# Kernel optimization log

Measured on AMD Instinct MI355X. Metric: run time of the kernel, lower is better.

## Reference

```python
import jax, jax.numpy as jnp
import numpy as np

N_NODES = 50000
N_EDGES = 1500000
FEAT = 128
CUTOFF = 5.0


def setup_inputs() -> dict:
    key = jax.random.key(0)
    k_x, k_ei, k_el, k_w = jax.random.split(key, 4)
    x = jax.random.normal(k_x, (N_NODES, FEAT), dtype=jnp.float32)
    edge_index = jax.random.randint(k_ei, (2, N_EDGES), 0, N_NODES, dtype=jnp.int64)
    edge_len = jax.random.uniform(k_el, (N_EDGES,), dtype=jnp.float32) * CUTOFF
    # learned params: equivariant mix (dense linear for scalar irreps, no bias),
    # log of distance scale (init sharpness=6.0), and 1->1 filter linear.
    W_mix = jax.random.normal(k_w, (FEAT, FEAT), dtype=jnp.float32) / np.sqrt(FEAT)
    log_scale = jnp.asarray(np.log(6.0), dtype=jnp.float32)
    filter_w = jnp.asarray(0.7, dtype=jnp.float32)
    filter_b = jnp.asarray(0.1, dtype=jnp.float32)
    return {"x": x, "edge_index": edge_index, "edge_len": edge_len,
            "W_mix": W_mix, "log_scale": log_scale,
            "filter_w": filter_w, "filter_b": filter_b}


def reference(x, edge_index, edge_len, W_mix, log_scale, filter_w, filter_b):
    sender = edge_index[0]
    receiver = edge_index[1]
    n_nodes = x.shape[0]

    scale = jnp.exp(log_scale).astype(edge_len.dtype)
    decay = jnp.exp(-jnp.maximum(edge_len / (scale + 1e-6), 0.0) ** 2)  # [E]
    gate = jax.nn.sigmoid(edge_len * filter_w + filter_b)               # [E]
    weights = jnp.nan_to_num(decay * gate, nan=0.0, posinf=0.0, neginf=0.0)

    # gather-scale-scatter: messages [E, F] -> per-node sum
    messages = weights[:, None].astype(x.dtype) * x[sender]
    agg = jax.ops.segment_sum(messages, receiver, num_segments=n_nodes)
    degree = jax.ops.segment_sum(jnp.ones_like(edge_len), receiver,
                                 num_segments=n_nodes)
    agg = agg / jnp.maximum(degree, 1.0)[:, None].astype(x.dtype)

    return x + agg @ W_mix
```

## Files before the change

kernel.cpp:

```cpp
#include <hip/hip_runtime.h>
#include <math.h>

#define FEAT 128
#define BSHIFT 5
#define BNODES 32
#define CAP 2048
#define NBUCK_MAX 2048

__device__ __forceinline__ float edge_weight(float d, float scale, float fw, float fb) {
    float t = fmaxf(d / scale, 0.0f);
    float decay = expf(-t * t);
    float g = 1.0f / (1.0f + expf(-(d * fw + fb)));
    float w = decay * g;
    if (!isfinite(w)) w = 0.0f;
    return w;
}

__device__ __forceinline__ unsigned int bf16_rne(float f) {
    unsigned int b = __float_as_uint(f);
    return (b + 0x7FFFu + ((b >> 16) & 1u)) >> 16;
}

__global__ __launch_bounds__(256) void convert_kernel(const float4* __restrict__ x4,
                                                      uint2* __restrict__ xbf,
                                                      int n4) {
    int i = blockIdx.x * 256 + threadIdx.x;
    if (i >= n4) return;
    float4 v = x4[i];
    uint2 o;
    o.x = (bf16_rne(v.y) << 16) | bf16_rne(v.x);
    o.y = (bf16_rne(v.w) << 16) | bf16_rne(v.z);
    xbf[i] = o;
}

__global__ __launch_bounds__(256) void count_kernel(const int* __restrict__ recv,
                                                    int* __restrict__ sub,
                                                    int E, int nbuck, int epb) {
    __shared__ int cnt[NBUCK_MAX];
    int tid = threadIdx.x;
    for (int i = tid; i < nbuck; i += 256) cnt[i] = 0;
    __syncthreads();
    int base = blockIdx.x * epb;
    int end = min(base + epb, E);
    for (int e = base + tid; e < end; e += 256)
        atomicAdd(&cnt[recv[e] >> BSHIFT], 1);
    __syncthreads();
    size_t row = (size_t)blockIdx.x * nbuck;
    for (int i = tid; i < nbuck; i += 256) sub[row + i] = cnt[i];
}

__global__ __launch_bounds__(256) void colscan_kernel(int* __restrict__ sub,
                                                      int* __restrict__ tot,
                                                      int nbuck, int nchunk) {
    __shared__ int vals[256];
    int b = blockIdx.x;
    int tid = threadIdx.x;
    int carry = 0;
    for (int c0 = 0; c0 < nchunk; c0 += 256) {
        int c = c0 + tid;
        int v = (c < nchunk) ? sub[(size_t)c * nbuck + b] : 0;
        vals[tid] = v;
        __syncthreads();
        for (int d = 1; d < 256; d <<= 1) {
            int t = (tid >= d) ? vals[tid - d] : 0;
            __syncthreads();
            vals[tid] += t;
            __syncthreads();
        }
        int excl = vals[tid] - v;
        if (c < nchunk) sub[(size_t)c * nbuck + b] = carry + excl;
        int btot = vals[255];
        __syncthreads();
        carry += btot;
    }
    if (tid == 0) tot[b] = carry;
}

__global__ __launch_bounds__(1024) void scan_kernel(const int* __restrict__ tot,
                                                    int* __restrict__ boff, int M) {
    __shared__ int part[1024];
    int t = threadIdx.x;
    int chunk = (M + 1023) >> 10;
    int lo = t * chunk, hi = min(lo + chunk, M);
    int s = 0;
    for (int i = lo; i < hi; ++i) s += tot[i];
    part[t] = s;
    __syncthreads();
    for (int d = 1; d < 1024; d <<= 1) {
        int v = (t >= d) ? part[t - d] : 0;
        __syncthreads();
        part[t] += v;
        __syncthreads();
    }
    int run = part[t] - s;
    for (int i = lo; i < hi; ++i) {
        boff[i] = run;
        run += tot[i];
    }
    if (hi == M) boff[M] = run;
}

__global__ __launch_bounds__(256) void bucket_scatter_kernel(
    const int* __restrict__ sender, const int* __restrict__ recv,
    const float* __restrict__ edge_len,
    const float* __restrict__ log_scale, const float* __restrict__ filter_w,
    const float* __restrict__ filter_b,
    const int* __restrict__ sub, const int* __restrict__ boff,
    unsigned long long* __restrict__ buf, int E, int nbuck, int epb) {
    __shared__ int cur[NBUCK_MAX];
    int tid = threadIdx.x;
    size_t row = (size_t)blockIdx.x * nbuck;
    for (int i = tid; i < nbuck; i += 256) cur[i] = boff[i] + sub[row + i];
    __syncthreads();
    int base = blockIdx.x * epb;
    int end = min(base + epb, E);
    float scale = expf(log_scale[0]) + 1e-6f;
    float fw = filter_w[0], fb = filter_b[0];
    for (int e = base + tid; e < end; e += 256) {
        int r = recv[e];
        int s = sender[e];
        float w = edge_weight(edge_len[e], scale, fw, fb);
        int pos = atomicAdd(&cur[r >> BSHIFT], 1);
        unsigned long long rec = ((unsigned long long)__float_as_uint(w) << 32)
                               | (unsigned int)(s & 0xFFFF)
                               | ((unsigned int)(r & (BNODES - 1)) << 16);
        buf[pos] = rec;
    }
}

__device__ __forceinline__ void accum8(float acc[8], uint4 u, float w) {
    acc[0] = fmaf(w, __uint_as_float(u.x << 16), acc[0]);
    acc[1] = fmaf(w, __uint_as_float(u.x & 0xFFFF0000u), acc[1]);
    acc[2] = fmaf(w, __uint_as_float(u.y << 16), acc[2]);
    acc[3] = fmaf(w, __uint_as_float(u.y & 0xFFFF0000u), acc[3]);
    acc[4] = fmaf(w, __uint_as_float(u.z << 16), acc[4]);
    acc[5] = fmaf(w, __uint_as_float(u.z & 0xFFFF0000u), acc[5]);
    acc[6] = fmaf(w, __uint_as_float(u.w << 16), acc[6]);
    acc[7] = fmaf(w, __uint_as_float(u.w & 0xFFFF0000u), acc[7]);
}

__global__ __launch_bounds__(256) void bucket_sort_aggregate_kernel(
    const uint4* __restrict__ xbf4, const unsigned long long* __restrict__ buf,
    const int* __restrict__ boff, uint4* __restrict__ agg_bf4,
    int* __restrict__ deg, int N) {
    __shared__ unsigned long long recS[CAP];
    __shared__ int cnt32[BNODES];
    __shared__ int segoff[BNODES + 1];

    int b = blockIdx.x;
    int n0 = b << BSHIFT;
    int nEnd = min(n0 + BNODES, N);
    int lo = boff[b], hi = boff[b + 1];
    int tid = threadIdx.x;
    int lane = tid & 15;
    int grp = tid >> 4;

    float acc[2][8] = {{0.f,0.f,0.f,0.f,0.f,0.f,0.f,0.f},
                       {0.f,0.f,0.f,0.f,0.f,0.f,0.f,0.f}};
    int dcnt[2] = {0, 0};

    for (int pos = lo; pos < hi; pos += CAP) {
        int cnt = min(CAP, hi - pos);
        if (tid < BNODES) cnt32[tid] = 0;
        __syncthreads();

        unsigned long long rec[CAP / 256];
        int rnk[CAP / 256];
        int locl[CAP / 256];
#pragma unroll
        for (int k = 0; k < CAP / 256; ++k) {
            int i = k * 256 + tid;
            if (i < cnt) {
                unsigned long long r = buf[pos + i];
                int l = ((unsigned int)r >> 16) & (BNODES - 1);
                rec[k] = r;
                locl[k] = l;
                rnk[k] = atomicAdd(&cnt32[l], 1);
            }
        }
        __syncthreads();
        if (tid == 0) {
            int run = 0;
#pragma unroll
            for (int l = 0; l < BNODES; ++l) { segoff[l] = run; run += cnt32[l]; }
            segoff[BNODES] = run;
        }
        __syncthreads();
#pragma unroll
        for (int k = 0; k < CAP / 256; ++k) {
            int i = k * 256 + tid;
            if (i < cnt) recS[segoff[locl[k]] + rnk[k]] = rec[k];
        }
        __syncthreads();

#pragma unroll
        for (int which = 0; which < 2; ++which) {
            int l = grp + which * 16;
            int s0 = segoff[l], s1 = segoff[l + 1];
            dcnt[which] += s1 - s0;
            int i = s0;
            for (; i + 4 <= s1; i += 4) {
                unsigned long long r0 = recS[i];
                unsigned long long r1 = recS[i + 1];
                unsigned long long r2 = recS[i + 2];
                unsigned long long r3 = recS[i + 3];
                float w0 = __uint_as_float((unsigned int)(r0 >> 32));
                float w1 = __uint_as_float((unsigned int)(r1 >> 32));
                float w2 = __uint_as_float((unsigned int)(r2 >> 32));
                float w3 = __uint_as_float((unsigned int)(r3 >> 32));
                int s0i = (unsigned int)r0 & 0xFFFF;
                int s1i = (unsigned int)r1 & 0xFFFF;
                int s2i = (unsigned int)r2 & 0xFFFF;
                int s3i = (unsigned int)r3 & 0xFFFF;
                uint4 u0 = xbf4[(size_t)s0i * 16 + lane];
                uint4 u1 = xbf4[(size_t)s1i * 16 + lane];
                uint4 u2 = xbf4[(size_t)s2i * 16 + lane];
                uint4 u3 = xbf4[(size_t)s3i * 16 + lane];
                accum8(acc[which], u0, w0);
                accum8(acc[which], u1, w1);
                accum8(acc[which], u2, w2);
                accum8(acc[which], u3, w3);
            }
            for (; i < s1; ++i) {
                unsigned long long ra = recS[i];
                float wa = __uint_as_float((unsigned int)(ra >> 32));
                int sa = (unsigned int)ra & 0xFFFF;
                uint4 ua = xbf4[(size_t)sa * 16 + lane];
                accum8(acc[which], ua, wa);
            }
        }
        __syncthreads();
    }

#pragma unroll
    for (int which = 0; which < 2; ++which) {
        int n = n0 + grp + which * 16;
        if (n < nEnd) {
            uint4 o;
            o.x = (bf16_rne(acc[which][1]) << 16) | bf16_rne(acc[which][0]);
            o.y = (bf16_rne(acc[which][3]) << 16) | bf16_rne(acc[which][2]);
            o.z = (bf16_rne(acc[which][5]) << 16) | bf16_rne(acc[which][4]);
            o.w = (bf16_rne(acc[which][7]) << 16) | bf16_rne(acc[which][6]);
            agg_bf4[(size_t)n * 16 + lane] = o;
            if (lane == 0) deg[n] = dcnt[which];
        }
    }
}

__global__ __launch_bounds__(256) void finalize_kernel(
    const float* __restrict__ x, const uint4* __restrict__ agg_bf4,
    const int* __restrict__ deg, const float* __restrict__ Wm,
    float* __restrict__ out, int N) {
    __shared__ float aggS[64 * 128];
    __shared__ float Ws[128 * 64];
    const int n0 = blockIdx.x * 64;

    for (int i = threadIdx.x; i < 64 * 16; i += 256) {
        int r = i >> 4;
        int q = i & 15;
        int n = n0 + r;
        uint4 u = make_uint4(0u, 0u, 0u, 0u);
        if (n < N) u = agg_bf4[(size_t)n * 16 + q];
        float4 f0, f1;
        f0.x = __uint_as_float(u.x << 16);
        f0.y = __uint_as_float(u.x & 0xFFFF0000u);
        f0.z = __uint_as_float(u.y << 16);
        f0.w = __uint_as_float(u.y & 0xFFFF0000u);
        f1.x = __uint_as_float(u.z << 16);
        f1.y = __uint_as_float(u.z & 0xFFFF0000u);
        f1.z = __uint_as_float(u.w << 16);
        f1.w = __uint_as_float(u.w & 0xFFFF0000u);
        int m = (r >> 2) & 7;
        ((float4*)aggS)[r * 32 + ((2 * q) ^ m)] = f0;
        ((float4*)aggS)[r * 32 + ((2 * q + 1) ^ m)] = f1;
    }

    const int tc = threadIdx.x & 15;
    const int tr = threadIdx.x >> 4;

    float invd[4];
#pragma unroll
    for (int i = 0; i < 4; ++i) {
        int n = n0 + 4 * tr + i;
        float degf = 1.0f;
        if (n < N) degf = fmaxf((float)deg[n], 1.0f);
        invd[i] = 1.0f / degf;
    }

    for (int h = 0; h < 2; ++h) {
        for (int i = threadIdx.x; i < 128 * 16; i += 256) {
            int k = i >> 4;
            int j4 = i & 15;
            ((float4*)Ws)[k * 16 + j4] = ((const float4*)Wm)[k * 32 + h * 16 + j4];
        }
        __syncthreads();

        float acc[4][4];
#pragma unroll
        for (int i = 0; i < 4; ++i)
#pragma unroll
            for (int c = 0; c < 4; ++c) acc[i][c] = 0.f;

#pragma unroll 4
        for (int k0 = 0; k0 < 128; k0 += 4) {
            float4 ar4[4];
            const int chunk = (k0 >> 2) ^ (tr & 7);
#pragma unroll
            for (int i = 0; i < 4; ++i) {
                int r = 4 * tr + i;
                ar4[i] = ((const float4*)aggS)[r * 32 + chunk];
            }
            float4 wv4[4];
#pragma unroll
            for (int kk = 0; kk < 4; ++kk)
                wv4[kk] = *(const float4*)&Ws[(k0 + kk) * 64 + tc * 4];

            float wvv[4][4];
#pragma unroll
            for (int kk = 0; kk < 4; ++kk) {
                wvv[kk][0] = wv4[kk].x; wvv[kk][1] = wv4[kk].y;
                wvv[kk][2] = wv4[kk].z; wvv[kk][3] = wv4[kk].w;
            }
#pragma unroll
            for (int i = 0; i < 4; ++i) {
                float av[4] = {ar4[i].x, ar4[i].y, ar4[i].z, ar4[i].w};
#pragma unroll
                for (int kk = 0; kk < 4; ++kk)
#pragma unroll
                    for (int c = 0; c < 4; ++c)
                        acc[i][c] = fmaf(av[kk], wvv[kk][c], acc[i][c]);
            }
        }

#pragma unroll
        for (int i = 0; i < 4; ++i) {
            int n = n0 + 4 * tr + i;
            if (n < N) {
                size_t base = (size_t)n * FEAT + h * 64 + tc * 4;
                float4 xv = *(const float4*)&x[base];
                float4 o;
                o.x = xv.x + invd[i] * acc[i][0];
                o.y = xv.y + invd[i] * acc[i][1];
                o.z = xv.z + invd[i] * acc[i][2];
                o.w = xv.w + invd[i] * acc[i][3];
                *(float4*)&out[base] = o;
            }
        }
        __syncthreads();
    }
}

__global__ __launch_bounds__(256) void scatter_fallback(
    const float4* __restrict__ x4, const int* __restrict__ sender,
    const int* __restrict__ receiver, const float* __restrict__ edge_len,
    const float* __restrict__ log_scale, const float* __restrict__ filter_w,
    const float* __restrict__ filter_b, float* __restrict__ agg,
    float* __restrict__ deg, int E) {
    int gid = blockIdx.x * 256 + threadIdx.x;
    int e = gid >> 5;
    if (e >= E) return;
    int lane = gid & 31;
    int s = sender[e];
    int r = receiver[e];
    float scale = expf(log_scale[0]) + 1e-6f;
    float w = edge_weight(edge_len[e], scale, filter_w[0], filter_b[0]);
    float4 xv = x4[s * (FEAT / 4) + lane];
    float* dst = agg + (size_t)r * FEAT + lane * 4;
    unsafeAtomicAdd(dst + 0, w * xv.x);
    unsafeAtomicAdd(dst + 1, w * xv.y);
    unsafeAtomicAdd(dst + 2, w * xv.z);
    unsafeAtomicAdd(dst + 3, w * xv.w);
    if (lane == 0) unsafeAtomicAdd(&deg[r], 1.0f);
}

__global__ __launch_bounds__(256) void finalize_fallback(
    const float* __restrict__ x, const float* __restrict__ agg,
    const float* __restrict__ deg, const float* __restrict__ Wm,
    float* __restrict__ out, int N) {
    __shared__ float Wsf[FEAT * FEAT];
    for (int i = threadIdx.x * 4; i < FEAT * FEAT; i += 256 * 4)
        *(float4*)&Wsf[i] = *(const float4*)&Wm[i];
    __syncthreads();
    int half = threadIdx.x >> 7;
    int j = threadIdx.x & (FEAT - 1);
    for (int n0 = blockIdx.x * 2; n0 < N; n0 += gridDim.x * 2) {
        int n = n0 + half;
        if (n < N) {
            const float* arow = agg + (size_t)n * FEAT;
            float acc = 0.0f;
#pragma unroll 16
            for (int k = 0; k < FEAT; ++k) acc = fmaf(arow[k], Wsf[k * FEAT + j], acc);
            float invd = 1.0f / fmaxf(deg[n], 1.0f);
            size_t idx = (size_t)n * FEAT + j;
            out[idx] = x[idx] + invd * acc;
        }
    }
}

extern "C" void kernel_launch(void* const* d_in, const int* in_sizes, int n_in,
                              void* d_out, int out_size, void* d_ws, size_t ws_size,
                              hipStream_t stream) {
    const float* x         = (const float*)d_in[0];
    const int*   ei        = (const int*)d_in[1];
    const float* edge_len  = (const float*)d_in[2];
    const float* W_mix     = (const float*)d_in[3];
    const float* log_scale = (const float*)d_in[4];
    const float* filter_w  = (const float*)d_in[5];
    const float* filter_b  = (const float*)d_in[6];
    float* out = (float*)d_out;

    const int N = in_sizes[0] / FEAT;
    const int E = in_sizes[1] / 2;
    const int* sender   = ei;
    const int* receiver = ei + E;
    const int nbuck = (N + BNODES - 1) >> BSHIFT;

    size_t xbf_bytes  = (size_t)N * FEAT * 2;
    size_t aggb_bytes = (size_t)N * FEAT * 2;
    size_t buf_bytes  = (size_t)E * 8;
    size_t tot_bytes  = (((size_t)nbuck * 4) + 63) & ~(size_t)63;
    size_t boff_bytes = (((size_t)(nbuck + 1) * 4) + 63) & ~(size_t)63;
    size_t deg_bytes  = (((size_t)N * 4) + 63) & ~(size_t)63;
    size_t fixed = xbf_bytes + aggb_bytes + buf_bytes + tot_bytes + boff_bytes +
                   deg_bytes;

    int epb = 0, nchunk = 0;
    size_t sub_bytes = 0;
    const int epb_opts[3] = {4096, 8192, 16384};
    for (int oi = 0; oi < 3; ++oi) {
        int cand = epb_opts[oi];
        int nc = (E + cand - 1) / cand;
        size_t sb = (((size_t)nc * nbuck * 4) + 63) & ~(size_t)63;
        if (fixed + sb <= ws_size) { epb = cand; nchunk = nc; sub_bytes = sb; break; }
    }

    if (epb != 0 && N <= 65536) {
        char* p = (char*)d_ws;
        uint2* xbf    = (uint2*)p;                        p += xbf_bytes;
        uint4* agg_bf = (uint4*)p;                        p += aggb_bytes;
        unsigned long long* buf = (unsigned long long*)p; p += buf_bytes;
        int* sub  = (int*)p;                              p += sub_bytes;
        int* tot  = (int*)p;                              p += tot_bytes;
        int* boff = (int*)p;                              p += boff_bytes;
        int* deg  = (int*)p;

        int cblocks = (N * (FEAT / 4) + 255) / 256;
        convert_kernel<<<cblocks, 256, 0, stream>>>((const float4*)x, xbf,
                                                    N * (FEAT / 4));
        count_kernel<<<nchunk, 256, 0, stream>>>(receiver, sub, E, nbuck, epb);
        colscan_kernel<<<nbuck, 256, 0, stream>>>(sub, tot, nbuck, nchunk);
        scan_kernel<<<1, 1024, 0, stream>>>(tot, boff, nbuck);
        bucket_scatter_kernel<<<nchunk, 256, 0, stream>>>(
            sender, receiver, edge_len, log_scale, filter_w, filter_b,
            sub, boff, buf, E, nbuck, epb);
        bucket_sort_aggregate_kernel<<<nbuck, 256, 0, stream>>>(
            (const uint4*)xbf, buf, boff, agg_bf, deg, N);
        int fblocks = (N + 63) / 64;
        finalize_kernel<<<fblocks, 256, 0, stream>>>(x, (const uint4*)agg_bf, deg,
                                                     W_mix, out, N);
    } else {
        float* agg = (float*)d_ws;
        float* degf = agg + (size_t)N * FEAT;
        hipMemsetAsync(agg, 0, ((size_t)N * FEAT + N) * sizeof(float), stream);
        int sblocks = (E * 32 + 255) / 256;
        scatter_fallback<<<sblocks, 256, 0, stream>>>(
            (const float4*)x, sender, receiver, edge_len,
            log_scale, filter_w, filter_b, agg, degf, E);
        finalize_fallback<<<512, 256, 0, stream>>>(x, agg, degf, W_mix, out, N);
    }
}
```

Baseline: 235.3 us.

## Halve bucket size to 16 nodes and merge convert and count kernels

Buckets now hold 16 receiver nodes instead of 32, which doubles the number of aggregate blocks. Each 16-lane group handles a single node, so the two-node accumulator loop goes away and occupancy and parallelism rise. The bf16 conversion and the receiver-count pass now run as one launch with block-index dispatch, which removes one kernel launch. The cost is twice as many buckets, which makes the per-chunk sub-count matrix, the colscan and the scan larger, and the count kernel now holds a 16KB shared histogram.

```diff
diff --git a/kernel.cpp b/kernel.cpp
--- a/kernel.cpp
+++ b/kernel.cpp
@@ -2,10 +2,10 @@
 #include <math.h>
 
 #define FEAT 128
-#define BSHIFT 5
-#define BNODES 32
-#define CAP 2048
-#define NBUCK_MAX 2048
+#define BSHIFT 4
+#define BNODES 16
+#define CAP 1024
+#define NBUCK_MAX 4096
 
 __device__ __forceinline__ float edge_weight(float d, float scale, float fw, float fb) {
     float t = fmaxf(d / scale, 0.0f);
@@ -21,31 +21,31 @@
     return (b + 0x7FFFu + ((b >> 16) & 1u)) >> 16;
 }
 
-__global__ __launch_bounds__(256) void convert_kernel(const float4* __restrict__ x4,
-                                                      uint2* __restrict__ xbf,
-                                                      int n4) {
-    int i = blockIdx.x * 256 + threadIdx.x;
-    if (i >= n4) return;
-    float4 v = x4[i];
-    uint2 o;
-    o.x = (bf16_rne(v.y) << 16) | bf16_rne(v.x);
-    o.y = (bf16_rne(v.w) << 16) | bf16_rne(v.z);
-    xbf[i] = o;
-}
-
-__global__ __launch_bounds__(256) void count_kernel(const int* __restrict__ recv,
-                                                    int* __restrict__ sub,
-                                                    int E, int nbuck, int epb) {
+__global__ __launch_bounds__(256) void convert_count_kernel(
+    const float4* __restrict__ x4, uint2* __restrict__ xbf, int n4,
+    const int* __restrict__ recv, int* __restrict__ sub,
+    int E, int nbuck, int epb, int cblocks) {
     __shared__ int cnt[NBUCK_MAX];
+    if ((int)blockIdx.x < cblocks) {
+        int i = blockIdx.x * 256 + threadIdx.x;
+        if (i >= n4) return;
+        float4 v = x4[i];
+        uint2 o;
+        o.x = (bf16_rne(v.y) << 16) | bf16_rne(v.x);
+        o.y = (bf16_rne(v.w) << 16) | bf16_rne(v.z);
+        xbf[i] = o;
+        return;
+    }
+    int cb = blockIdx.x - cblocks;
     int tid = threadIdx.x;
     for (int i = tid; i < nbuck; i += 256) cnt[i] = 0;
     __syncthreads();
-    int base = blockIdx.x * epb;
+    int base = cb * epb;
     int end = min(base + epb, E);
     for (int e = base + tid; e < end; e += 256)
         atomicAdd(&cnt[recv[e] >> BSHIFT], 1);
     __syncthreads();
-    size_t row = (size_t)blockIdx.x * nbuck;
+    size_t row = (size_t)cb * nbuck;
     for (int i = tid; i < nbuck; i += 256) sub[row + i] = cnt[i];
 }
 
@@ -144,7 +144,7 @@
     const int* __restrict__ boff, uint4* __restrict__ agg_bf4,
     int* __restrict__ deg, int N) {
     __shared__ unsigned long long recS[CAP];
-    __shared__ int cnt32[BNODES];
+    __shared__ int cnt16[BNODES];
     __shared__ int segoff[BNODES + 1];
 
     int b = blockIdx.x;
@@ -155,13 +155,12 @@
     int lane = tid & 15;
     int grp = tid >> 4;
 
-    float acc[2][8] = {{0.f,0.f,0.f,0.f,0.f,0.f,0.f,0.f},
-                       {0.f,0.f,0.f,0.f,0.f,0.f,0.f,0.f}};
-    int dcnt[2] = {0, 0};
+    float acc[8] = {0.f,0.f,0.f,0.f,0.f,0.f,0.f,0.f};
+    int dcnt = 0;
 
     for (int pos = lo; pos < hi; pos += CAP) {
         int cnt = min(CAP, hi - pos);
-        if (tid < BNODES) cnt32[tid] = 0;
+        if (tid < BNODES) cnt16[tid] = 0;
         __syncthreads();
 
         unsigned long long rec[CAP / 256];
@@ -175,14 +174,14 @@
                 int l = ((unsigned int)r >> 16) & (BNODES - 1);
                 rec[k] = r;
                 locl[k] = l;
-                rnk[k] = atomicAdd(&cnt32[l], 1);
+                rnk[k] = atomicAdd(&cnt16[l], 1);
             }
         }
         __syncthreads();
         if (tid == 0) {
             int run = 0;
 #pragma unroll
-            for (int l = 0; l < BNODES; ++l) { segoff[l] = run; run += cnt32[l]; }
+            for (int l = 0; l < BNODES; ++l) { segoff[l] = run; run += cnt16[l]; }
             segoff[BNODES] = run;
         }
         __syncthreads();
@@ -193,11 +192,9 @@
         }
         __syncthreads();
 
-#pragma unroll
-        for (int which = 0; which < 2; ++which) {
-            int l = grp + which * 16;
-            int s0 = segoff[l], s1 = segoff[l + 1];
-            dcnt[which] += s1 - s0;
+        {
+            int s0 = segoff[grp], s1 = segoff[grp + 1];
+            dcnt += s1 - s0;
             int i = s0;
             for (; i + 4 <= s1; i += 4) {
                 unsigned long long r0 = recS[i];
@@ -216,33 +213,32 @@
                 uint4 u1 = xbf4[(size_t)s1i * 16 + lane];
                 uint4 u2 = xbf4[(size_t)s2i * 16 + lane];
                 uint4 u3 = xbf4[(size_t)s3i * 16 + lane];
-                accum8(acc[which], u0, w0);
-                accum8(acc[which], u1, w1);
-                accum8(acc[which], u2, w2);
-                accum8(acc[which], u3, w3);
+                accum8(acc, u0, w0);
+                accum8(acc, u1, w1);
+                accum8(acc, u2, w2);
+                accum8(acc, u3, w3);
             }
             for (; i < s1; ++i) {
                 unsigned long long ra = recS[i];
                 float wa = __uint_as_float((unsigned int)(ra >> 32));
                 int sa = (unsigned int)ra & 0xFFFF;
                 uint4 ua = xbf4[(size_t)sa * 16 + lane];
-                accum8(acc[which], ua, wa);
-            }
-        }
-        __syncthreads();
-    }
-
-#pragma unroll
-    for (int which = 0; which < 2; ++which) {
-        int n = n0 + grp + which * 16;
+                accum8(acc, ua, wa);
+            }
+        }
+        __syncthreads();
+    }
+
+    {
+        int n = n0 + grp;
         if (n < nEnd) {
             uint4 o;
-            o.x = (bf16_rne(acc[which][1]) << 16) | bf16_rne(acc[which][0]);
-            o.y = (bf16_rne(acc[which][3]) << 16) | bf16_rne(acc[which][2]);
-            o.z = (bf16_rne(acc[which][5]) << 16) | bf16_rne(acc[which][4]);
-            o.w = (bf16_rne(acc[which][7]) << 16) | bf16_rne(acc[which][6]);
+            o.x = (bf16_rne(acc[1]) << 16) | bf16_rne(acc[0]);
+            o.y = (bf16_rne(acc[3]) << 16) | bf16_rne(acc[2]);
+            o.z = (bf16_rne(acc[5]) << 16) | bf16_rne(acc[4]);
+            o.w = (bf16_rne(acc[7]) << 16) | bf16_rne(acc[6]);
             agg_bf4[(size_t)n * 16 + lane] = o;
-            if (lane == 0) deg[n] = dcnt[which];
+            if (lane == 0) deg[n] = dcnt;
         }
     }
 }
@@ -445,9 +441,9 @@
         int* deg  = (int*)p;
 
         int cblocks = (N * (FEAT / 4) + 255) / 256;
-        convert_kernel<<<cblocks, 256, 0, stream>>>((const float4*)x, xbf,
-                                                    N * (FEAT / 4));
-        count_kernel<<<nchunk, 256, 0, stream>>>(receiver, sub, E, nbuck, epb);
+        convert_count_kernel<<<cblocks + nchunk, 256, 0, stream>>>(
+            (const float4*)x, xbf, N * (FEAT / 4),
+            receiver, sub, E, nbuck, epb, cblocks);
         colscan_kernel<<<nbuck, 256, 0, stream>>>(sub, tot, nbuck, nchunk);
         scan_kernel<<<1, 1024, 0, stream>>>(tot, boff, nbuck);
         bucket_scatter_kernel<<<nchunk, 256, 0, stream>>>(
```

Measured after the change: 238.6 us. No clear change (+1.4%).
